# Optimization experiments

Hardware: AMD Instinct MI355X
Metric: run time of the kernel (lower is better)

Reference implementation:

```python
import jax, jax.numpy as jnp
import numpy as np

N_NODES = 50000
IN_CH, HID_CH, OUT_CH = 128, 128, 64
N_EDGES = 800000


def setup_inputs() -> dict:
    key = jax.random.key(0)
    k = jax.random.split(key, 6)
    x = jax.random.normal(k[0], (N_NODES, IN_CH), dtype=jnp.float32)
    edge_index = jax.random.randint(k[1], (2, N_EDGES), 0, N_NODES, dtype=jnp.int64)
    # Glorot-ish init for weights
    W1 = jax.random.normal(k[2], (IN_CH, HID_CH), dtype=jnp.float32) * (1.0 / np.sqrt(IN_CH))
    b1 = jnp.zeros((HID_CH,), dtype=jnp.float32)
    W2 = jax.random.normal(k[3], (HID_CH, OUT_CH), dtype=jnp.float32) * (1.0 / np.sqrt(HID_CH))
    b2 = jnp.zeros((OUT_CH,), dtype=jnp.float32)
    return {"x": x, "edge_index": edge_index, "W1": W1, "b1": b1, "W2": W2, "b2": b2}


def _gcn_conv(x, src, dst, W, b, n_nodes):
    """PyG GCNConv: linear, add self-loops, symmetric deg^-1/2 normalization, scatter-add."""
    h = x @ W  # [N, F_out]
    loop = jnp.arange(n_nodes, dtype=src.dtype)
    s = jnp.concatenate([src, loop])  # [E+N]
    d = jnp.concatenate([dst, loop])
    # in-degree on target nodes (including self-loops), edge weight = 1
    deg = jnp.zeros((n_nodes,), dtype=h.dtype).at[d].add(1.0)
    dinv = jnp.where(deg > 0, jax.lax.rsqrt(deg), 0.0)
    norm = dinv[s] * dinv[d]  # [E+N]
    msg = h[s] * norm[:, None]  # [E+N, F_out]
    out = jax.ops.segment_sum(msg, d, num_segments=n_nodes)
    return out + b


def reference(x, edge_index, W1, b1, W2, b2):
    src, dst = edge_index[0], edge_index[1]
    h = _gcn_conv(x, src, dst, W1, b1, N_NODES)
    h = jax.nn.relu(h)
    # dropout in eval mode -> identity
    out = _gcn_conv(h, src, dst, W2, b2, N_NODES)
    return out
```

## Files before the change

### kernel.cpp

```cpp
#include <hip/hip_runtime.h>

typedef __attribute__((ext_vector_type(8))) short bf16x8;
typedef __attribute__((ext_vector_type(4))) float f32x4;

constexpr int NN = 50000;
constexpr int NE = 800000;
constexpr int C1 = 128;
constexpr int C2 = 64;
constexpr int NBK = 196;
constexpr int EPB = 2048;
constexpr int NBLK = (NE + EPB - 1) / EPB;
constexpr int MT = NN / 16;
constexpr int MMB = 250;
constexpr int MMWAVES = MMB * 4;

__device__ __forceinline__ unsigned short f2bf(float f) {
    unsigned int u = __float_as_uint(f);
    u += 0x7FFFu + ((u >> 16) & 1u);
    return (unsigned short)(u >> 16);
}
__device__ __forceinline__ float2 bf2f(unsigned int u) {
    return make_float2(__uint_as_float(u << 16), __uint_as_float(u & 0xFFFF0000u));
}
__device__ __forceinline__ bf16x8 pack8(float4 a, float4 b) {
    bf16x8 r;
    r[0] = (short)f2bf(a.x); r[1] = (short)f2bf(a.y);
    r[2] = (short)f2bf(a.z); r[3] = (short)f2bf(a.w);
    r[4] = (short)f2bf(b.x); r[5] = (short)f2bf(b.y);
    r[6] = (short)f2bf(b.z); r[7] = (short)f2bf(b.w);
    return r;
}
__device__ __forceinline__ void addrow(float* a, uint4 v) {
    float2 p;
    p = bf2f(v.x); a[0] += p.x; a[1] += p.y;
    p = bf2f(v.y); a[2] += p.x; a[3] += p.y;
    p = bf2f(v.z); a[4] += p.x; a[5] += p.y;
    p = bf2f(v.w); a[6] += p.x; a[7] += p.y;
}

__global__ __launch_bounds__(256) void bin_kernel(const int* __restrict__ src,
                                                  const int* __restrict__ dst,
                                                  unsigned int* __restrict__ ebuf,
                                                  int* __restrict__ localOff,
                                                  int* __restrict__ bktHist) {
    __shared__ int lhist[NBK];
    __shared__ int ls[256];
    __shared__ int lcur[NBK];
    __shared__ unsigned int lbuf[EPB];
    const int t = threadIdx.x;
    const int base = blockIdx.x * EPB;
    if (t < NBK) lhist[t] = 0;
    __syncthreads();
    int b[8]; unsigned int p[8];
    #pragma unroll
    for (int i = 0; i < 8; i++) {
        int e = base + i * 256 + t;
        if (e < NE) {
            int s = src[e], d = dst[e];
            b[i] = d >> 8;
            p[i] = ((unsigned int)(d & 255) << 16) | (unsigned int)s;
            atomicAdd(&lhist[b[i]], 1);
        } else b[i] = -1;
    }
    __syncthreads();
    int v = (t < NBK) ? lhist[t] : 0;
    ls[t] = v;
    __syncthreads();
    #pragma unroll
    for (int d = 1; d < 256; d <<= 1) {
        int u = (t >= d) ? ls[t - d] : 0;
        __syncthreads();
        ls[t] += u;
        __syncthreads();
    }
    if (t < NBK) {
        int ex = ls[t] - v;
        lcur[t] = ex;
        localOff[blockIdx.x * 200 + t] = ex;
        if (v > 0) atomicAdd(&bktHist[t], v);
    }
    if (t == NBK - 1) localOff[blockIdx.x * 200 + NBK] = ls[t];
    __syncthreads();
    #pragma unroll
    for (int i = 0; i < 8; i++) {
        if (b[i] >= 0) {
            int lp = atomicAdd(&lcur[b[i]], 1);
            lbuf[lp] = p[i];
        }
    }
    __syncthreads();
    #pragma unroll
    for (int i = 0; i < 8; i++)
        ebuf[base + i * 256 + t] = lbuf[i * 256 + t];
}

__global__ __launch_bounds__(256) void place_kernel(const unsigned int* __restrict__ ebuf,
                                                    const int* __restrict__ localOff,
                                                    const int* __restrict__ bktHist,
                                                    unsigned short* __restrict__ esrc,
                                                    int* __restrict__ cnt,
                                                    int* __restrict__ off,
                                                    float* __restrict__ dinv) {
    __shared__ int lhist[256];
    __shared__ int ls[256];
    __shared__ int lcur[256];
    __shared__ int sSegBase;
    const int t = threadIdx.x;
    const int bkt = blockIdx.x;
    const int node0 = bkt << 8;
    const int nnodes = min(256, NN - node0);
    int v0 = (t < NBK) ? bktHist[t] : 0;
    ls[t] = v0;
    __syncthreads();
    #pragma unroll
    for (int d = 1; d < 256; d <<= 1) {
        int u = (t >= d) ? ls[t - d] : 0;
        __syncthreads();
        ls[t] += u;
        __syncthreads();
    }
    if (t == bkt) sSegBase = ls[t] - v0;
    lhist[t] = 0;
    __syncthreads();
    for (int j = t; j < NBLK; j += 256) {
        int s = localOff[j * 200 + bkt];
        int e = localOff[j * 200 + bkt + 1];
        const unsigned int* q = ebuf + j * EPB;
        for (int k = s; k < e; k++) atomicAdd(&lhist[q[k] >> 16], 1);
    }
    __syncthreads();
    int v = lhist[t];
    ls[t] = v;
    __syncthreads();
    #pragma unroll
    for (int d = 1; d < 256; d <<= 1) {
        int u = (t >= d) ? ls[t - d] : 0;
        __syncthreads();
        ls[t] += u;
        __syncthreads();
    }
    int ex = ls[t] - v;
    lcur[t] = ex;
    const int segBase = sSegBase;
    if (t < nnodes) {
        cnt[node0 + t] = v;
        off[node0 + t] = segBase + ex;
        dinv[node0 + t] = rsqrtf((float)v + 1.0f);
    }
    __syncthreads();
    for (int j = t; j < NBLK; j += 256) {
        int s = localOff[j * 200 + bkt];
        int e = localOff[j * 200 + bkt + 1];
        const unsigned int* q = ebuf + j * EPB;
        for (int k = s; k < e; k++) {
            unsigned int pp = q[k];
            int lp = atomicAdd(&lcur[pp >> 16], 1);
            esrc[segBase + lp] = (unsigned short)(pp & 0xFFFFu);
        }
    }
}

__global__ __launch_bounds__(256, 2) void mm1_kernel(const float* __restrict__ x,
                                                     const float* __restrict__ W,
                                                     const float* __restrict__ dinv,
                                                     unsigned short* __restrict__ g1) {
    __shared__ unsigned short wl[4][8][64][8];
    const int t = threadIdx.x;
    for (int i = 0; i < 64; i++) {
        int idx = i * 256 + t;
        int k = idx >> 7, n = idx & 127;
        wl[k >> 5][n >> 4][((k >> 3) & 3) * 16 + (n & 15)][k & 7] = f2bf(W[idx]);
    }
    __syncthreads();
    const int lane = t & 63, lm = lane & 15, quad = lane >> 4;

    bf16x8 bfr[4][8];
    #pragma unroll
    for (int s = 0; s < 4; s++)
        #pragma unroll
        for (int nt = 0; nt < 8; nt++)
            bfr[s][nt] = *(const bf16x8*)&wl[s][nt][lane][0];

    int wg = blockIdx.x * 4 + (t >> 6);
    for (int tile = wg; tile < MT; tile += MMWAVES) {
        int row0 = tile << 4;
        const float* xr = x + (size_t)(row0 + lm) * 128 + quad * 8;
        bf16x8 af[4];
        #pragma unroll
        for (int s = 0; s < 4; s++) {
            float4 p = *(const float4*)(xr + s * 32);
            float4 q = *(const float4*)(xr + s * 32 + 4);
            af[s] = pack8(p, q);
        }
        f32x4 acc[8];
        #pragma unroll
        for (int nt = 0; nt < 8; nt++) acc[nt] = (f32x4){0.f, 0.f, 0.f, 0.f};
        #pragma unroll
        for (int s = 0; s < 4; s++)
            #pragma unroll
            for (int nt = 0; nt < 8; nt++)
                acc[nt] = __builtin_amdgcn_mfma_f32_16x16x32_bf16(af[s], bfr[s][nt],
                                                                  acc[nt], 0, 0, 0);
        float4 dv = *(const float4*)(dinv + row0 + quad * 4);
        float dvv[4] = {dv.x, dv.y, dv.z, dv.w};
        #pragma unroll
        for (int nt = 0; nt < 8; nt++)
            #pragma unroll
            for (int r = 0; r < 4; r++)
                g1[(size_t)(row0 + quad * 4 + r) * 128 + nt * 16 + lm] =
                    f2bf(acc[nt][r] * dvv[r]);
    }
}

__global__ __launch_bounds__(256, 2) void mm2_kernel(const unsigned short* __restrict__ x2,
                                                     const float* __restrict__ W,
                                                     const float* __restrict__ dinv,
                                                     unsigned short* __restrict__ g2) {
    __shared__ unsigned short wl[4][4][64][8];
    const int t = threadIdx.x;
    for (int i = 0; i < 32; i++) {
        int idx = i * 256 + t;
        int k = idx >> 6, n = idx & 63;
        wl[k >> 5][n >> 4][((k >> 3) & 3) * 16 + (n & 15)][k & 7] = f2bf(W[idx]);
    }
    __syncthreads();
    const int lane = t & 63, lm = lane & 15, quad = lane >> 4;

    bf16x8 bfr[4][4];
    #pragma unroll
    for (int s = 0; s < 4; s++)
        #pragma unroll
        for (int nt = 0; nt < 4; nt++)
            bfr[s][nt] = *(const bf16x8*)&wl[s][nt][lane][0];

    int wg = blockIdx.x * 4 + (t >> 6);
    for (int tile = wg; tile < MT; tile += MMWAVES) {
        int row0 = tile << 4;
        const bf16x8* xr = (const bf16x8*)(x2 + (size_t)(row0 + lm) * 128 + quad * 8);
        bf16x8 af[4];
        #pragma unroll
        for (int s = 0; s < 4; s++) af[s] = xr[s * 4];
        f32x4 acc[4];
        #pragma unroll
        for (int nt = 0; nt < 4; nt++) acc[nt] = (f32x4){0.f, 0.f, 0.f, 0.f};
        #pragma unroll
        for (int s = 0; s < 4; s++)
            #pragma unroll
            for (int nt = 0; nt < 4; nt++)
                acc[nt] = __builtin_amdgcn_mfma_f32_16x16x32_bf16(af[s], bfr[s][nt],
                                                                  acc[nt], 0, 0, 0);
        float4 dv = *(const float4*)(dinv + row0 + quad * 4);
        float dvv[4] = {dv.x, dv.y, dv.z, dv.w};
        #pragma unroll
        for (int nt = 0; nt < 4; nt++)
            #pragma unroll
            for (int r = 0; r < 4; r++)
                g2[(size_t)(row0 + quad * 4 + r) * 64 + nt * 16 + lm] =
                    f2bf(acc[nt][r] * dvv[r]);
    }
}

__global__ __launch_bounds__(256) void gather1_kernel(const unsigned short* __restrict__ g1,
                                                      const unsigned short* __restrict__ esrc,
                                                      const int* __restrict__ off,
                                                      const int* __restrict__ cnt,
                                                      const float* __restrict__ dinv,
                                                      const float* __restrict__ b1,
                                                      unsigned short* __restrict__ x2) {
    const int wave = threadIdx.x >> 6, lane = threadIdx.x & 63;
    const int slot = lane >> 4, part = lane & 15;
    int n = blockIdx.x * 4 + wave;
    if (n >= NN) return;
    const uint4* G = (const uint4*)g1;
    float a0[8] = {0,0,0,0,0,0,0,0};
    float a1[8] = {0,0,0,0,0,0,0,0};
    if (slot == 0) addrow(a0, G[(size_t)n * 16 + part]);
    int s0 = off[n], c = cnt[n];
    int i = slot;
    for (; i + 4 < c; i += 8) {
        int sA = esrc[s0 + i];
        int sB = esrc[s0 + i + 4];
        uint4 vA = G[(size_t)sA * 16 + part];
        uint4 vB = G[(size_t)sB * 16 + part];
        addrow(a0, vA);
        addrow(a1, vB);
    }
    if (i < c) addrow(a0, G[(size_t)esrc[s0 + i] * 16 + part]);
    #pragma unroll
    for (int j = 0; j < 8; j++) a0[j] += a1[j];
    #pragma unroll
    for (int j = 0; j < 8; j++) {
        a0[j] += __shfl_xor(a0[j], 16);
        a0[j] += __shfl_xor(a0[j], 32);
    }
    if (slot == 0) {
        float s = dinv[n];
        float4 bA = ((const float4*)b1)[part * 2];
        float4 bB = ((const float4*)b1)[part * 2 + 1];
        float4 p = make_float4(fmaxf(s * a0[0] + bA.x, 0.f), fmaxf(s * a0[1] + bA.y, 0.f),
                               fmaxf(s * a0[2] + bA.z, 0.f), fmaxf(s * a0[3] + bA.w, 0.f));
        float4 q = make_float4(fmaxf(s * a0[4] + bB.x, 0.f), fmaxf(s * a0[5] + bB.y, 0.f),
                               fmaxf(s * a0[6] + bB.z, 0.f), fmaxf(s * a0[7] + bB.w, 0.f));
        *(bf16x8*)(x2 + (size_t)n * 128 + part * 8) = pack8(p, q);
    }
}

__global__ __launch_bounds__(256) void gather2_kernel(const unsigned short* __restrict__ g2,
                                                      const unsigned short* __restrict__ esrc,
                                                      const int* __restrict__ off,
                                                      const int* __restrict__ cnt,
                                                      const float* __restrict__ dinv,
                                                      const float* __restrict__ b2,
                                                      float* __restrict__ out) {
    const int wave = threadIdx.x >> 6, lane = threadIdx.x & 63;
    const int slot = lane >> 3, part = lane & 7;
    int n = blockIdx.x * 4 + wave;
    if (n >= NN) return;
    const uint4* G = (const uint4*)g2;
    float a0[8] = {0,0,0,0,0,0,0,0};
    float a1[8] = {0,0,0,0,0,0,0,0};
    if (slot == 0) addrow(a0, G[(size_t)n * 8 + part]);
    int s0 = off[n], c = cnt[n];
    int i = slot;
    for (; i + 8 < c; i += 16) {
        int sA = esrc[s0 + i];
        int sB = esrc[s0 + i + 8];
        uint4 vA = G[(size_t)sA * 8 + part];
        uint4 vB = G[(size_t)sB * 8 + part];
        addrow(a0, vA);
        addrow(a1, vB);
    }
    if (i < c) addrow(a0, G[(size_t)esrc[s0 + i] * 8 + part]);
    #pragma unroll
    for (int j = 0; j < 8; j++) a0[j] += a1[j];
    #pragma unroll
    for (int j = 0; j < 8; j++) {
        a0[j] += __shfl_xor(a0[j], 8);
        a0[j] += __shfl_xor(a0[j], 16);
        a0[j] += __shfl_xor(a0[j], 32);
    }
    if (slot == 0) {
        float s = dinv[n];
        float4 bA = ((const float4*)b2)[part * 2];
        float4 bB = ((const float4*)b2)[part * 2 + 1];
        float* o = out + (size_t)n * 64 + part * 8;
        *(float4*)o = make_float4(s * a0[0] + bA.x, s * a0[1] + bA.y,
                                  s * a0[2] + bA.z, s * a0[3] + bA.w);
        *(float4*)(o + 4) = make_float4(s * a0[4] + bB.x, s * a0[5] + bB.y,
                                        s * a0[6] + bB.z, s * a0[7] + bB.w);
    }
}

extern "C" void kernel_launch(void* const* d_in, const int* in_sizes, int n_in,
                              void* d_out, int out_size, void* d_ws, size_t ws_size,
                              hipStream_t stream) {
    const float* x  = (const float*)d_in[0];
    const int* edges = (const int*)d_in[1];
    const float* W1 = (const float*)d_in[2];
    const float* b1 = (const float*)d_in[3];
    const float* W2 = (const float*)d_in[4];
    const float* b2 = (const float*)d_in[5];
    const int* src = edges;
    const int* dst = edges + NE;

    int* bktHist   = (int*)d_ws;
    int* localOff  = bktHist + 208;
    unsigned int* ebuf = (unsigned int*)(localOff + 78208);
    unsigned short* esrc = (unsigned short*)(ebuf + (size_t)NBLK * EPB);
    int* cnt       = (int*)(esrc + 800768);
    int* off       = cnt + 50048;
    float* dinv    = (float*)(off + 50048);
    unsigned short* g1 = (unsigned short*)(dinv + 50048);
    unsigned short* x2 = g1 + (size_t)NN * C1;
    unsigned short* g2 = g1;
    float* out = (float*)d_out;

    hipMemsetAsync(bktHist, 0, 208 * sizeof(int), stream);

    bin_kernel<<<NBLK, 256, 0, stream>>>(src, dst, ebuf, localOff, bktHist);
    place_kernel<<<NBK, 256, 0, stream>>>(ebuf, localOff, bktHist, esrc, cnt, off, dinv);

    mm1_kernel<<<MMB, 256, 0, stream>>>(x, W1, dinv, g1);
    gather1_kernel<<<(NN + 3) / 4, 256, 0, stream>>>(g1, esrc, off, cnt, dinv, b1, x2);

    mm2_kernel<<<MMB, 256, 0, stream>>>(x2, W2, dinv, g2);
    gather2_kernel<<<(NN + 3) / 4, 256, 0, stream>>>(g2, esrc, off, cnt, dinv, b2, out);
}
```

Measured before the change: 206.5 us.

## Drop global bucket histogram, spread place loops over waves, unroll gather1 by four

The global bucket histogram, its memset and its atomics are removed. Each place block now computes its segment base by summing the per-block exclusive offsets across all bin blocks with a shared-memory tree reduction. The place kernel's counting and scatter loops change from one thread walking one bin-block segment to one wave per segment with lanes striding over its edges. This shortens the serial chain per thread but leaves most lanes idle, since segments hold only about ten edges, and it adds many more outer iterations per wave. gather1 now keeps four accumulator sets with four independent row loads in flight instead of two, to get more memory-level parallelism.

```diff
diff --git a/kernel.cpp b/kernel.cpp
--- a/kernel.cpp
+++ b/kernel.cpp
@@ -41,8 +41,7 @@
 __global__ __launch_bounds__(256) void bin_kernel(const int* __restrict__ src,
                                                   const int* __restrict__ dst,
                                                   unsigned int* __restrict__ ebuf,
-                                                  int* __restrict__ localOff,
-                                                  int* __restrict__ bktHist) {
+                                                  int* __restrict__ localOff) {
     __shared__ int lhist[NBK];
     __shared__ int ls[256];
     __shared__ int lcur[NBK];
@@ -74,10 +73,8 @@
         __syncthreads();
     }
     if (t < NBK) {
-        int ex = ls[t] - v;
-        lcur[t] = ex;
-        localOff[blockIdx.x * 200 + t] = ex;
-        if (v > 0) atomicAdd(&bktHist[t], v);
+        lcur[t] = ls[t] - v;
+        localOff[blockIdx.x * 200 + t] = ls[t] - v;
     }
     if (t == NBK - 1) localOff[blockIdx.x * 200 + NBK] = ls[t];
     __syncthreads();
@@ -96,7 +93,6 @@
 
 __global__ __launch_bounds__(256) void place_kernel(const unsigned int* __restrict__ ebuf,
                                                     const int* __restrict__ localOff,
-                                                    const int* __restrict__ bktHist,
                                                     unsigned short* __restrict__ esrc,
                                                     int* __restrict__ cnt,
                                                     int* __restrict__ off,
@@ -104,29 +100,30 @@
     __shared__ int lhist[256];
     __shared__ int ls[256];
     __shared__ int lcur[256];
-    __shared__ int sSegBase;
+    __shared__ int red[256];
     const int t = threadIdx.x;
+    const int wv = t >> 6, ln = t & 63;
     const int bkt = blockIdx.x;
     const int node0 = bkt << 8;
     const int nnodes = min(256, NN - node0);
-    int v0 = (t < NBK) ? bktHist[t] : 0;
-    ls[t] = v0;
-    __syncthreads();
-    #pragma unroll
-    for (int d = 1; d < 256; d <<= 1) {
-        int u = (t >= d) ? ls[t - d] : 0;
-        __syncthreads();
-        ls[t] += u;
-        __syncthreads();
-    }
-    if (t == bkt) sSegBase = ls[t] - v0;
+
+    int part = 0;
+    for (int j = t; j < NBLK; j += 256) part += localOff[j * 200 + bkt];
+    red[t] = part;
     lhist[t] = 0;
     __syncthreads();
-    for (int j = t; j < NBLK; j += 256) {
+    #pragma unroll
+    for (int d = 128; d > 0; d >>= 1) {
+        if (t < d) red[t] += red[t + d];
+        __syncthreads();
+    }
+    const int segBase = red[0];
+
+    for (int j = wv; j < NBLK; j += 4) {
         int s = localOff[j * 200 + bkt];
         int e = localOff[j * 200 + bkt + 1];
         const unsigned int* q = ebuf + j * EPB;
-        for (int k = s; k < e; k++) atomicAdd(&lhist[q[k] >> 16], 1);
+        for (int k = s + ln; k < e; k += 64) atomicAdd(&lhist[q[k] >> 16], 1);
     }
     __syncthreads();
     int v = lhist[t];
@@ -141,18 +138,17 @@
     }
     int ex = ls[t] - v;
     lcur[t] = ex;
-    const int segBase = sSegBase;
     if (t < nnodes) {
         cnt[node0 + t] = v;
         off[node0 + t] = segBase + ex;
         dinv[node0 + t] = rsqrtf((float)v + 1.0f);
     }
     __syncthreads();
-    for (int j = t; j < NBLK; j += 256) {
+    for (int j = wv; j < NBLK; j += 4) {
         int s = localOff[j * 200 + bkt];
         int e = localOff[j * 200 + bkt + 1];
         const unsigned int* q = ebuf + j * EPB;
-        for (int k = s; k < e; k++) {
+        for (int k = s + ln; k < e; k += 64) {
             unsigned int pp = q[k];
             int lp = atomicAdd(&lcur[pp >> 16], 1);
             esrc[segBase + lp] = (unsigned short)(pp & 0xFFFFu);
@@ -274,20 +270,28 @@
     const uint4* G = (const uint4*)g1;
     float a0[8] = {0,0,0,0,0,0,0,0};
     float a1[8] = {0,0,0,0,0,0,0,0};
+    float a2[8] = {0,0,0,0,0,0,0,0};
+    float a3[8] = {0,0,0,0,0,0,0,0};
     if (slot == 0) addrow(a0, G[(size_t)n * 16 + part]);
     int s0 = off[n], c = cnt[n];
     int i = slot;
-    for (; i + 4 < c; i += 8) {
+    for (; i + 12 < c; i += 16) {
         int sA = esrc[s0 + i];
         int sB = esrc[s0 + i + 4];
+        int sC = esrc[s0 + i + 8];
+        int sD = esrc[s0 + i + 12];
         uint4 vA = G[(size_t)sA * 16 + part];
         uint4 vB = G[(size_t)sB * 16 + part];
+        uint4 vC = G[(size_t)sC * 16 + part];
+        uint4 vD = G[(size_t)sD * 16 + part];
         addrow(a0, vA);
         addrow(a1, vB);
-    }
-    if (i < c) addrow(a0, G[(size_t)esrc[s0 + i] * 16 + part]);
-    #pragma unroll
-    for (int j = 0; j < 8; j++) a0[j] += a1[j];
+        addrow(a2, vC);
+        addrow(a3, vD);
+    }
+    for (; i < c; i += 4) addrow(a0, G[(size_t)esrc[s0 + i] * 16 + part]);
+    #pragma unroll
+    for (int j = 0; j < 8; j++) a0[j] += a1[j] + a2[j] + a3[j];
     #pragma unroll
     for (int j = 0; j < 8; j++) {
         a0[j] += __shfl_xor(a0[j], 16);
@@ -363,8 +367,7 @@
     const int* src = edges;
     const int* dst = edges + NE;
 
-    int* bktHist   = (int*)d_ws;
-    int* localOff  = bktHist + 208;
+    int* localOff  = (int*)d_ws;
     unsigned int* ebuf = (unsigned int*)(localOff + 78208);
     unsigned short* esrc = (unsigned short*)(ebuf + (size_t)NBLK * EPB);
     int* cnt       = (int*)(esrc + 800768);
@@ -375,10 +378,8 @@
     unsigned short* g2 = g1;
     float* out = (float*)d_out;
 
-    hipMemsetAsync(bktHist, 0, 208 * sizeof(int), stream);
-
-    bin_kernel<<<NBLK, 256, 0, stream>>>(src, dst, ebuf, localOff, bktHist);
-    place_kernel<<<NBK, 256, 0, stream>>>(ebuf, localOff, bktHist, esrc, cnt, off, dinv);
+    bin_kernel<<<NBLK, 256, 0, stream>>>(src, dst, ebuf, localOff);
+    place_kernel<<<NBK, 256, 0, stream>>>(ebuf, localOff, esrc, cnt, off, dinv);
 
     mm1_kernel<<<MMB, 256, 0, stream>>>(x, W1, dinv, g1);
     gather1_kernel<<<(NN + 3) / 4, 256, 0, stream>>>(g1, esrc, off, cnt, dinv, b1, x2);
```

Result: slower. 265.6 us (+28.6%).
